# Performance work log

Measured on AMD Instinct MI355X. Metric: run time of the kernel, lower is better.

## Reference

```python
import jax, jax.numpy as jnp
import numpy as np

T, B, C, H, L = 384, 48, 256, 256, 2


def setup_inputs() -> dict:
    key = jax.random.key(0)
    ks = jax.random.split(key, 8)
    s = 1.0 / np.sqrt(H)  # torch GRUCell uniform(-1/sqrt(H), 1/sqrt(H)) init
    xav = np.sqrt(2.0 / (H + 1))  # xavier_normal_ for the [1,H] skip-gate linear
    return {
        "x": jax.random.normal(ks[0], (T, B, C), jnp.float32),
        "hiddens": jax.random.normal(ks[1], (L, 1, H), jnp.float32),
        "w_ih": jax.random.uniform(ks[2], (L, 3 * H, C), jnp.float32, -s, s),
        "w_hh": jax.random.uniform(ks[3], (L, 3 * H, H), jnp.float32, -s, s),
        "b_ih": jax.random.uniform(ks[4], (L, 3 * H), jnp.float32, -s, s),
        "b_hh": jax.random.uniform(ks[5], (L, 3 * H), jnp.float32, -s, s),
        "lw": jax.random.normal(ks[6], (L, 1, H), jnp.float32) * xav,
        "lb": jnp.ones((L, 1), jnp.float32),  # linear.bias.data.fill_(1)
    }


def _ste(v):
    # straight-through round: forward round, backward identity
    return v + jax.lax.stop_gradient(jnp.round(v) - v)


def reference(x, hiddens, w_ih, w_hh, b_ih, b_hh, lw, lb):
    Tn, Bn, _ = x.shape
    Ln, _, Hn = hiddens.shape
    skip = jnp.zeros((Bn,), dtype=bool)          # carried across layers (as in torch loop)
    du = jnp.zeros((Bn, 1), x.dtype)             # delta_u, carried across layers
    inp = x
    hs, bus = [], []
    for i in range(Ln):
        wi, wh, bi, bh = w_ih[i], w_hh[i], b_ih[i], b_hh[i]
        lwi, lbi = lw[i], lb[i]
        h0 = jnp.broadcast_to(hiddens[i], (Bn, Hn))  # h.repeat(1, bs, 1)
        u0 = jnp.ones((Bn, 1), x.dtype)              # u reset per layer

        def step(carry, x_t):
            h, u, skp, d = carry
            bu = _ste(u)                                  # [B,1]
            # GRUCell: gates order (r, z, n)
            gi = x_t @ wi.T + bi                          # [B,3H]
            gh = h @ wh.T + bh                            # [B,3H]
            i_r, i_z, i_n = jnp.split(gi, 3, axis=1)
            h_r, h_z, h_n = jnp.split(gh, 3, axis=1)
            r = jax.nn.sigmoid(i_r + h_r)
            z = jax.nn.sigmoid(i_z + h_z)
            n = jnp.tanh(i_n + r * h_n)
            cand = (1.0 - z) * n + z * h
            # non-skip branch
            h_ns = cand * bu
            d_ns = jax.nn.sigmoid(h_ns @ lwi.T + lbi)     # [B,1]
            s = skp[:, None]
            new_h = jnp.where(s, h * (1.0 - bu), h_ns)
            new_d = jnp.where(s, d, d_ns)
            new_u = jnp.where(s, jnp.clip(u + d, 0.0, 1.0) * (1.0 - bu), d_ns * bu)
            # n_skips_after = ceil(0.5/new_u) - 1 ; skip if > 0 (non-diff path)
            nsa = jnp.ceil(0.5 / jax.lax.stop_gradient(new_u)) - 1.0
            new_skip = nsa[:, 0] > 0
            return (new_h, new_u, new_skip, new_d), (new_h, bu)

        (h_f, _, skip, du), (ys, bu_seq) = jax.lax.scan(step, (h0, u0, skip, du), inp)
        inp = ys                 # [T,B,H] feeds next layer
        hs.append(h_f)           # final hidden [B,H]
        bus.append(bu_seq)       # [T,B,1]
    out = inp
    hs = jnp.stack(hs, axis=0)                                   # [L,B,H]
    total_u = jnp.concatenate([b[:, :, 0].T for b in bus], 1)    # [B, L*T]
    return (out, hs, total_u)
```

## Files before the change

### kernel.cpp

```cpp
#include <hip/hip_runtime.h>
#include <stdint.h>


#define T_STEPS 384
#define BATCH   48
#define HID     256

__device__ __forceinline__ float sigm_(float x) { return 1.f / (1.f + __expf(-x)); }
__device__ __forceinline__ float tanh_(float x) {
    float ax = fabsf(x);
    float e  = __expf(-2.f * ax);
    float r  = (1.f - e) / (1.f + e);
    return copysignf(r, x);
}

__global__ __launch_bounds__(256, 2) void gemm_nt(const float* __restrict__ X,
                                                  const float* __restrict__ W,
                                                  const float* __restrict__ B,
                                                  float* __restrict__ O)
{
    __shared__ float As[32 * 140];
    __shared__ float Bs[32 * 68];

    const int tid = threadIdx.x;
    const int tx  = tid & 15;
    const int ty  = tid >> 4;
    const int n0  = blockIdx.x * 64;
    const int m0  = blockIdx.y * 128;

    float acc[8][4];
#pragma unroll
    for (int i = 0; i < 8; ++i)
#pragma unroll
        for (int j = 0; j < 4; ++j) acc[i][j] = 0.f;

    const float4 bias4 = *reinterpret_cast<const float4*>(B + n0 + tx * 4);

    for (int kc = 0; kc < 8; ++kc) {
        const int k0 = kc * 32;
        float4 a[4], bb[2];
#pragma unroll
        for (int j = 0; j < 4; ++j) {
            int f = tid + 256 * j, r = f >> 3, cq = f & 7;
            a[j] = *reinterpret_cast<const float4*>(X + (size_t)(m0 + r) * 256 + k0 + cq * 4);
        }
#pragma unroll
        for (int j = 0; j < 2; ++j) {
            int f = tid + 256 * j, r = f >> 3, cq = f & 7;
            bb[j] = *reinterpret_cast<const float4*>(W + (size_t)(n0 + r) * 256 + k0 + cq * 4);
        }
        __syncthreads();
#pragma unroll
        for (int j = 0; j < 4; ++j) {
            int f = tid + 256 * j, r = f >> 3, cq = f & 7;
            As[(cq * 4 + 0) * 140 + r] = a[j].x;
            As[(cq * 4 + 1) * 140 + r] = a[j].y;
            As[(cq * 4 + 2) * 140 + r] = a[j].z;
            As[(cq * 4 + 3) * 140 + r] = a[j].w;
        }
#pragma unroll
        for (int j = 0; j < 2; ++j) {
            int f = tid + 256 * j, r = f >> 3, cq = f & 7;
            Bs[(cq * 4 + 0) * 68 + r] = bb[j].x;
            Bs[(cq * 4 + 1) * 68 + r] = bb[j].y;
            Bs[(cq * 4 + 2) * 68 + r] = bb[j].z;
            Bs[(cq * 4 + 3) * 68 + r] = bb[j].w;
        }
        __syncthreads();
#pragma unroll 8
        for (int kk = 0; kk < 32; ++kk) {
            float4 av0 = *reinterpret_cast<const float4*>(As + kk * 140 + ty * 8);
            float4 av1 = *reinterpret_cast<const float4*>(As + kk * 140 + ty * 8 + 4);
            float4 bv  = *reinterpret_cast<const float4*>(Bs + kk * 68 + tx * 4);
            float am[8] = {av0.x, av0.y, av0.z, av0.w, av1.x, av1.y, av1.z, av1.w};
            float bn[4] = {bv.x, bv.y, bv.z, bv.w};
#pragma unroll
            for (int i = 0; i < 8; ++i)
#pragma unroll
                for (int j = 0; j < 4; ++j) acc[i][j] = fmaf(am[i], bn[j], acc[i][j]);
        }
    }
#pragma unroll
    for (int i = 0; i < 8; ++i) {
        int row = m0 + ty * 8 + i;
        float4 o;
        o.x = acc[i][0] + bias4.x;
        o.y = acc[i][1] + bias4.y;
        o.z = acc[i][2] + bias4.z;
        o.w = acc[i][3] + bias4.w;
        *reinterpret_cast<float4*>(O + (size_t)row * 768 + n0 + tx * 4) = o;
    }
}

__global__ __launch_bounds__(512, 2) void rec_layer(
    const float* __restrict__ GI, float* __restrict__ Yout,
    const float* __restrict__ whh, const float* __restrict__ bhh,
    const float* __restrict__ lwl, const float* __restrict__ lbl,
    const float* __restrict__ hid,
    unsigned long long* XH, unsigned long long* PD,
    float* __restrict__ hsout, float* __restrict__ tuout)
{
    __shared__ float hbuf[2112];
    __shared__ float pdw[2][8];

    const int tid  = threadIdx.x;
    const int lane = tid & 63;
    const int w    = tid >> 6;
    const int g    = lane & 15;
    const int s    = lane >> 4;
    const int b    = blockIdx.x % 48;
    const int p    = blockIdx.x / 48;
    const int q    = 1 - p;
    const int cb   = w * 16 + g;
    const int c    = p * 128 + cb;

    float4 WrO[8], WzO[8], WnO[8], WrP[8], WzP[8], WnP[8];
    {
        const size_t rR = (size_t)c * 256;
        const size_t rZ = (size_t)(256 + c) * 256;
        const size_t rN = (size_t)(512 + c) * 256;
        const int ko = p * 128 + s * 32;
        const int kq = q * 128 + s * 32;
        const float4* a  = reinterpret_cast<const float4*>(whh + rR + ko);
        const float4* bv = reinterpret_cast<const float4*>(whh + rZ + ko);
        const float4* cv = reinterpret_cast<const float4*>(whh + rN + ko);
        const float4* d4 = reinterpret_cast<const float4*>(whh + rR + kq);
        const float4* e4 = reinterpret_cast<const float4*>(whh + rZ + kq);
        const float4* f4 = reinterpret_cast<const float4*>(whh + rN + kq);
#pragma unroll
        for (int i = 0; i < 8; ++i) {
            WrO[i] = a[i];  WzO[i] = bv[i]; WnO[i] = cv[i];
            WrP[i] = d4[i]; WzP[i] = e4[i]; WnP[i] = f4[i];
        }
    }

    const float bhr = bhh[c], bhz = bhh[256 + c], bhn = bhh[512 + c];
    const float lwc = lwl[c];
    const float lbv = lbl[0];

    if (tid < 256) {
        float v = hid[tid];
        hbuf[tid] = v; hbuf[264 + tid] = v; hbuf[528 + tid] = v; hbuf[792 + tid] = v;
    }
    __syncthreads();

    float gir, giz, gin;
    {
        const size_t g0 = (size_t)b * 768 + c;
        gir = GI[g0]; giz = GI[g0 + 256]; gin = GI[g0 + 512];
    }
    float sAr, sAz, sAn;
    {
        float ar = 0.f, az = 0.f, an = 0.f;
        const float4* ho = reinterpret_cast<const float4*>(hbuf + s * 264 + p * 128 + s * 32);
        const float4* hq = reinterpret_cast<const float4*>(hbuf + s * 264 + q * 128 + s * 32);
#pragma unroll
        for (int i = 0; i < 8; ++i) {
            float4 hv = ho[i];
            ar = fmaf(WrO[i].x, hv.x, ar); ar = fmaf(WrO[i].y, hv.y, ar);
            ar = fmaf(WrO[i].z, hv.z, ar); ar = fmaf(WrO[i].w, hv.w, ar);
            az = fmaf(WzO[i].x, hv.x, az); az = fmaf(WzO[i].y, hv.y, az);
            az = fmaf(WzO[i].z, hv.z, az); az = fmaf(WzO[i].w, hv.w, az);
            an = fmaf(WnO[i].x, hv.x, an); an = fmaf(WnO[i].y, hv.y, an);
            an = fmaf(WnO[i].z, hv.z, an); an = fmaf(WnO[i].w, hv.w, an);
        }
#pragma unroll
        for (int i = 0; i < 8; ++i) {
            float4 hv = hq[i];
            ar = fmaf(WrP[i].x, hv.x, ar); ar = fmaf(WrP[i].y, hv.y, ar);
            ar = fmaf(WrP[i].z, hv.z, ar); ar = fmaf(WrP[i].w, hv.w, ar);
            az = fmaf(WzP[i].x, hv.x, az); az = fmaf(WzP[i].y, hv.y, az);
            az = fmaf(WzP[i].z, hv.z, az); az = fmaf(WzP[i].w, hv.w, az);
            an = fmaf(WnP[i].x, hv.x, an); an = fmaf(WnP[i].y, hv.y, an);
            an = fmaf(WnP[i].z, hv.z, an); an = fmaf(WnP[i].w, hv.w, an);
        }
        ar += __shfl_xor(ar, 16); ar += __shfl_xor(ar, 32);
        az += __shfl_xor(az, 16); az += __shfl_xor(az, 32);
        an += __shfl_xor(an, 16); an += __shfl_xor(an, 32);
        sAr = ar; sAz = az; sAn = an;
    }

    float u = 1.f, d = 0.f;
    bool  skip = false;
    int   ns = 0;
    int   hp = 0;

    unsigned long long* XHb = XH + b * 512;
    unsigned long long* PDb = PD + b * 4;

    for (int t = 0; t < T_STEPS; ++t) {
        const float bu  = rintf(u);
        const float obu = 1.f - bu;
        const size_t yrow = ((size_t)t * 48 + b) * 256;
        const int tp = (t < T_STEPS - 1) ? t + 1 : t;
        const size_t gpb = ((size_t)tp * 48 + b) * 768 + c;

        if (skip) {
            float* hb = hbuf + hp * 1056;
            float hcv = hb[s * 264 + c];
            float nh  = hcv * obu;
            if (bu != 0.f) hb[s * 264 + c] = nh;
            if (s == 1) {
                Yout[yrow + c] = nh;
                if (t == T_STEPS - 1) hsout[b * 256 + c] = nh;
            }
            if (bu != 0.f) { sAr = 0.f; sAz = 0.f; sAn = 0.f; }
            if (p == 0 && tid == 0) tuout[b * 768 + t] = bu;
            float pr = GI[gpb], pz = GI[gpb + 256], pn = GI[gpb + 512];
            u    = fminf(fmaxf(u + d, 0.f), 1.f) * obu;
            skip = (u < 0.5f);
            __syncthreads();
            gir = pr; giz = pz; gin = pn;
        } else {
            const int sl = ns & 1;
            const unsigned int tag = (unsigned int)ns + 1u;

            float hcv = hbuf[hp * 1056 + s * 264 + c];
            float rr  = sigm_(gir + sAr + bhr);
            float zz  = sigm_(giz + sAz + bhz);
            float tn  = tanh_(gin + rr * (sAn + bhn));
            float nh  = ((1.f - zz) * tn + zz * hcv) * bu;
            float pdv = nh * lwc;

            float* hbn = hbuf + (hp ^ 1) * 1056;
            hbn[s * 264 + c] = nh;
            if (s == 0) {
                unsigned long long pk0p = ((unsigned long long)tag << 32) |
                                          (unsigned long long)__float_as_uint(nh);
                __hip_atomic_store(XHb + sl * 256 + c, pk0p, __ATOMIC_RELAXED, __HIP_MEMORY_SCOPE_AGENT);
            } else if (s == 1) {
                Yout[yrow + c] = nh;
                if (t == T_STEPS - 1) hsout[b * 256 + c] = nh;
            }
            pdv += __shfl_xor(pdv, 1);  pdv += __shfl_xor(pdv, 2);  pdv += __shfl_xor(pdv, 4);
            pdv += __shfl_xor(pdv, 8);  pdv += __shfl_xor(pdv, 16); pdv += __shfl_xor(pdv, 32);
            pdv *= 0.25f;
            if (lane == 0) pdw[sl][w] = pdv;
            if (p == 0 && tid == 0) tuout[b * 768 + t] = bu;
            __syncthreads();

            float ownpd = ((pdw[sl][0] + pdw[sl][1]) + (pdw[sl][2] + pdw[sl][3]))
                        + ((pdw[sl][4] + pdw[sl][5]) + (pdw[sl][6] + pdw[sl][7]));
            if (tid == 0) {
                unsigned long long pkp = ((unsigned long long)tag << 32) |
                                         (unsigned long long)__float_as_uint(ownpd);
                __hip_atomic_store(PDb + sl * 2 + p, pkp, __ATOMIC_RELAXED, __HIP_MEMORY_SCOPE_AGENT);
            }
            unsigned long long pk0 =
                __hip_atomic_load(XHb + sl * 256 + q * 128 + cb, __ATOMIC_RELAXED, __HIP_MEMORY_SCOPE_AGENT);
            float pr = GI[gpb], pz = GI[gpb + 256], pn = GI[gpb + 512];

            float ar = 0.f, az = 0.f, an = 0.f;
            {
                const float4* ho = reinterpret_cast<const float4*>(hbn + s * 264 + p * 128 + s * 32);
#pragma unroll
                for (int i = 0; i < 8; ++i) {
                    float4 hv = ho[i];
                    ar = fmaf(WrO[i].x, hv.x, ar); ar = fmaf(WrO[i].y, hv.y, ar);
                    ar = fmaf(WrO[i].z, hv.z, ar); ar = fmaf(WrO[i].w, hv.w, ar);
                    az = fmaf(WzO[i].x, hv.x, az); az = fmaf(WzO[i].y, hv.y, az);
                    az = fmaf(WzO[i].z, hv.z, az); az = fmaf(WzO[i].w, hv.w, az);
                    an = fmaf(WnO[i].x, hv.x, an); an = fmaf(WnO[i].y, hv.y, an);
                    an = fmaf(WnO[i].z, hv.z, an); an = fmaf(WnO[i].w, hv.w, an);
                }
            }
            {
                const int qc = q * 128 + cb;
                const unsigned long long* slp = XHb + sl * 256 + qc;
                while ((unsigned int)(pk0 >> 32) < tag)
                    pk0 = __hip_atomic_load(slp, __ATOMIC_RELAXED, __HIP_MEMORY_SCOPE_AGENT);
                hbn[s * 264 + qc] = __uint_as_float((unsigned int)pk0);
            }
            __syncthreads();

            unsigned long long pkq = __hip_atomic_load(PDb + sl * 2 + q, __ATOMIC_RELAXED, __HIP_MEMORY_SCOPE_AGENT);

            {
                const float4* hq = reinterpret_cast<const float4*>(hbn + s * 264 + q * 128 + s * 32);
#pragma unroll
                for (int i = 0; i < 8; ++i) {
                    float4 hv = hq[i];
                    ar = fmaf(WrP[i].x, hv.x, ar); ar = fmaf(WrP[i].y, hv.y, ar);
                    ar = fmaf(WrP[i].z, hv.z, ar); ar = fmaf(WrP[i].w, hv.w, ar);
                    az = fmaf(WzP[i].x, hv.x, az); az = fmaf(WzP[i].y, hv.y, az);
                    az = fmaf(WzP[i].z, hv.z, az); az = fmaf(WzP[i].w, hv.w, az);
                    an = fmaf(WnP[i].x, hv.x, an); an = fmaf(WnP[i].y, hv.y, an);
                    an = fmaf(WnP[i].z, hv.z, an); an = fmaf(WnP[i].w, hv.w, an);
                }
            }
            ar += __shfl_xor(ar, 16); ar += __shfl_xor(ar, 32);
            az += __shfl_xor(az, 16); az += __shfl_xor(az, 32);
            an += __shfl_xor(an, 16); an += __shfl_xor(an, 32);
            sAr = ar; sAz = az; sAn = an;

            while ((unsigned int)(pkq >> 32) < tag)
                pkq = __hip_atomic_load(PDb + sl * 2 + q, __ATOMIC_RELAXED, __HIP_MEMORY_SCOPE_AGENT);
            const float pdq = __uint_as_float((unsigned int)pkq);

            float dns = sigm_((ownpd + pdq) + lbv);
            u = dns * bu; d = dns;
            skip = (u < 0.5f);
            ns++; hp ^= 1;
            gir = pr; giz = pz; gin = pn;
        }
    }
}

extern "C" void kernel_launch(void* const* d_in, const int* in_sizes, int n_in,
                              void* d_out, int out_size, void* d_ws, size_t ws_size,
                              hipStream_t stream)
{
    const float* x   = (const float*)d_in[0];
    const float* hid = (const float*)d_in[1];
    const float* wih = (const float*)d_in[2];
    const float* whh = (const float*)d_in[3];
    const float* bih = (const float*)d_in[4];
    const float* bhh = (const float*)d_in[5];
    const float* lw  = (const float*)d_in[6];
    const float* lb  = (const float*)d_in[7];
    float* out = (float*)d_out;

    float* ws = (float*)d_ws;
    float* GI = ws;
    float* Y0 = GI + (size_t)18432 * 768;
    unsigned long long* XH0 = (unsigned long long*)(Y0 + (size_t)18432 * 256);
    unsigned long long* XH1 = XH0 + 48 * 512;
    unsigned long long* PD0 = XH1 + 48 * 512;
    unsigned long long* PD1 = PD0 + 192;

    float* OUTy = out;
    float* HS   = out + (size_t)18432 * 256;
    float* TU   = HS + 2 * 48 * 256;

    hipMemsetAsync(XH0, 0, (size_t)(48 * 512 * 2 + 48 * 4 * 2) * sizeof(unsigned long long), stream);

    dim3 ggrid(12, 144), gblk(256);
    gemm_nt<<<ggrid, gblk, 0, stream>>>(x, wih, bih, GI);
    rec_layer<<<96, 512, 0, stream>>>(GI, Y0, whh, bhh, lw, lb, hid, XH0, PD0, HS, TU);
    gemm_nt<<<ggrid, gblk, 0, stream>>>(Y0, wih + 196608, bih + 768, GI);
    rec_layer<<<96, 512, 0, stream>>>(GI, OUTy, whh + 196608, bhh + 768, lw + 256, lb + 1,
                                      hid + 256, XH1, PD1, HS + 12288, TU + 384);
}
```

Before: 2.064 ms.

## Fuse both GRU layers into one wavefront-pipelined persistent kernel

Replaces the layer-1 recurrence, the layer-2 input GEMM and the layer-2 recurrence with a single persistent launch. Layer-1 blocks stream each hidden state through a 16-slot ring buffer, extra blocks compute the layer-2 input projection per step, and layer-2 blocks consume it, with tag-based atomic flags and progress counters providing flow control. This overlaps the two serial recurrences so their latency chains run concurrently instead of back to back. In exchange it needs all 208 blocks co-resident (risk of deadlock otherwise), adds spin-wait traffic, and computes the layer-2 GEMM per timestep at low efficiency.

```diff
diff --git a/kernel.cpp b/kernel.cpp
--- a/kernel.cpp
+++ b/kernel.cpp
@@ -3,8 +3,7 @@
 
 
 #define T_STEPS 384
-#define BATCH   48
-#define HID     256
+typedef unsigned long long u64t;
 
 __device__ __forceinline__ float sigm_(float x) { return 1.f / (1.f + __expf(-x)); }
 __device__ __forceinline__ float tanh_(float x) {
@@ -92,216 +91,375 @@
     }
 }
 
-__global__ __launch_bounds__(512, 2) void rec_layer(
-    const float* __restrict__ GI, float* __restrict__ Yout,
-    const float* __restrict__ whh, const float* __restrict__ bhh,
-    const float* __restrict__ lwl, const float* __restrict__ lbl,
-    const float* __restrict__ hid,
-    unsigned long long* XH, unsigned long long* PD,
-    float* __restrict__ hsout, float* __restrict__ tuout)
+__global__ __launch_bounds__(512, 2) void fused_pipe(
+    const float* __restrict__ GI1,
+    const float* __restrict__ wih2, const float* __restrict__ bih2,
+    const float* __restrict__ whh1, const float* __restrict__ bhh1,
+    const float* __restrict__ whh2, const float* __restrict__ bhh2,
+    const float* __restrict__ lw1, const float* __restrict__ lb1,
+    const float* __restrict__ lw2, const float* __restrict__ lb2,
+    const float* __restrict__ hid1, const float* __restrict__ hid2,
+    u64t* XH1, u64t* PD1, u64t* XH2, u64t* PD2,
+    u64t* Y1X, u64t* GI2X, unsigned int* BPROG, unsigned int* CPROG,
+    float* __restrict__ OUTy, float* __restrict__ HS, float* __restrict__ TU)
 {
     __shared__ float hbuf[2112];
     __shared__ float pdw[2][8];
+    __shared__ float ybuf[6336];
 
     const int tid  = threadIdx.x;
     const int lane = tid & 63;
     const int w    = tid >> 6;
     const int g    = lane & 15;
     const int s    = lane >> 4;
-    const int b    = blockIdx.x % 48;
-    const int p    = blockIdx.x / 48;
-    const int q    = 1 - p;
-    const int cb   = w * 16 + g;
-    const int c    = p * 128 + cb;
-
-    float4 WrO[8], WzO[8], WnO[8], WrP[8], WzP[8], WnP[8];
-    {
-        const size_t rR = (size_t)c * 256;
-        const size_t rZ = (size_t)(256 + c) * 256;
-        const size_t rN = (size_t)(512 + c) * 256;
-        const int ko = p * 128 + s * 32;
-        const int kq = q * 128 + s * 32;
-        const float4* a  = reinterpret_cast<const float4*>(whh + rR + ko);
-        const float4* bv = reinterpret_cast<const float4*>(whh + rZ + ko);
-        const float4* cv = reinterpret_cast<const float4*>(whh + rN + ko);
-        const float4* d4 = reinterpret_cast<const float4*>(whh + rR + kq);
-        const float4* e4 = reinterpret_cast<const float4*>(whh + rZ + kq);
-        const float4* f4 = reinterpret_cast<const float4*>(whh + rN + kq);
-#pragma unroll
-        for (int i = 0; i < 8; ++i) {
-            WrO[i] = a[i];  WzO[i] = bv[i]; WnO[i] = cv[i];
-            WrP[i] = d4[i]; WzP[i] = e4[i]; WnP[i] = f4[i];
-        }
-    }
-
-    const float bhr = bhh[c], bhz = bhh[256 + c], bhn = bhh[512 + c];
-    const float lwc = lwl[c];
-    const float lbv = lbl[0];
-
-    if (tid < 256) {
-        float v = hid[tid];
-        hbuf[tid] = v; hbuf[264 + tid] = v; hbuf[528 + tid] = v; hbuf[792 + tid] = v;
-    }
-    __syncthreads();
-
-    float gir, giz, gin;
-    {
-        const size_t g0 = (size_t)b * 768 + c;
-        gir = GI[g0]; giz = GI[g0 + 256]; gin = GI[g0 + 512];
-    }
-    float sAr, sAz, sAn;
-    {
-        float ar = 0.f, az = 0.f, an = 0.f;
-        const float4* ho = reinterpret_cast<const float4*>(hbuf + s * 264 + p * 128 + s * 32);
-        const float4* hq = reinterpret_cast<const float4*>(hbuf + s * 264 + q * 128 + s * 32);
-#pragma unroll
-        for (int i = 0; i < 8; ++i) {
-            float4 hv = ho[i];
-            ar = fmaf(WrO[i].x, hv.x, ar); ar = fmaf(WrO[i].y, hv.y, ar);
-            ar = fmaf(WrO[i].z, hv.z, ar); ar = fmaf(WrO[i].w, hv.w, ar);
-            az = fmaf(WzO[i].x, hv.x, az); az = fmaf(WzO[i].y, hv.y, az);
-            az = fmaf(WzO[i].z, hv.z, az); az = fmaf(WzO[i].w, hv.w, az);
-            an = fmaf(WnO[i].x, hv.x, an); an = fmaf(WnO[i].y, hv.y, an);
-            an = fmaf(WnO[i].z, hv.z, an); an = fmaf(WnO[i].w, hv.w, an);
-        }
-#pragma unroll
-        for (int i = 0; i < 8; ++i) {
-            float4 hv = hq[i];
-            ar = fmaf(WrP[i].x, hv.x, ar); ar = fmaf(WrP[i].y, hv.y, ar);
-            ar = fmaf(WrP[i].z, hv.z, ar); ar = fmaf(WrP[i].w, hv.w, ar);
-            az = fmaf(WzP[i].x, hv.x, az); az = fmaf(WzP[i].y, hv.y, az);
-            az = fmaf(WzP[i].z, hv.z, az); az = fmaf(WzP[i].w, hv.w, az);
-            an = fmaf(WnP[i].x, hv.x, an); an = fmaf(WnP[i].y, hv.y, an);
-            an = fmaf(WnP[i].z, hv.z, an); an = fmaf(WnP[i].w, hv.w, an);
-        }
-        ar += __shfl_xor(ar, 16); ar += __shfl_xor(ar, 32);
-        az += __shfl_xor(az, 16); az += __shfl_xor(az, 32);
-        an += __shfl_xor(an, 16); an += __shfl_xor(an, 32);
-        sAr = ar; sAz = az; sAn = an;
-    }
-
-    float u = 1.f, d = 0.f;
-    bool  skip = false;
-    int   ns = 0;
-    int   hp = 0;
-
-    unsigned long long* XHb = XH + b * 512;
-    unsigned long long* PDb = PD + b * 4;
-
-    for (int t = 0; t < T_STEPS; ++t) {
-        const float bu  = rintf(u);
-        const float obu = 1.f - bu;
-        const size_t yrow = ((size_t)t * 48 + b) * 256;
-        const int tp = (t < T_STEPS - 1) ? t + 1 : t;
-        const size_t gpb = ((size_t)tp * 48 + b) * 768 + c;
-
-        if (skip) {
-            float* hb = hbuf + hp * 1056;
-            float hcv = hb[s * 264 + c];
-            float nh  = hcv * obu;
-            if (bu != 0.f) hb[s * 264 + c] = nh;
-            if (s == 1) {
-                Yout[yrow + c] = nh;
-                if (t == T_STEPS - 1) hsout[b * 256 + c] = nh;
-            }
-            if (bu != 0.f) { sAr = 0.f; sAz = 0.f; sAn = 0.f; }
-            if (p == 0 && tid == 0) tuout[b * 768 + t] = bu;
-            float pr = GI[gpb], pz = GI[gpb + 256], pn = GI[gpb + 512];
-            u    = fminf(fmaxf(u + d, 0.f), 1.f) * obu;
-            skip = (u < 0.5f);
-            __syncthreads();
-            gir = pr; giz = pz; gin = pn;
+    const int blk  = blockIdx.x;
+
+    if (blk < 192) {
+        const bool isA = (blk < 96);
+        const int rb   = isA ? blk : (blk - 96);
+        const int b    = rb % 48;
+        const int p    = rb / 48;
+        const int q    = 1 - p;
+        const int cb   = w * 16 + g;
+        const int c    = p * 128 + cb;
+
+        const float* whh = isA ? whh1 : whh2;
+        const float* bhh = isA ? bhh1 : bhh2;
+        const float* lwl = isA ? lw1 : lw2;
+        const float* lbl = isA ? lb1 : lb2;
+        const float* hid = isA ? hid1 : hid2;
+        u64t* XHb = (isA ? XH1 : XH2) + b * 512;
+        u64t* PDb = (isA ? PD1 : PD2) + b * 4;
+
+        float4 WrO[8], WzO[8], WnO[8], WrP[8], WzP[8], WnP[8];
+        {
+            const size_t rR = (size_t)c * 256;
+            const size_t rZ = (size_t)(256 + c) * 256;
+            const size_t rN = (size_t)(512 + c) * 256;
+            const int ko = p * 128 + s * 32;
+            const int kq = q * 128 + s * 32;
+            const float4* a  = reinterpret_cast<const float4*>(whh + rR + ko);
+            const float4* bv = reinterpret_cast<const float4*>(whh + rZ + ko);
+            const float4* cv = reinterpret_cast<const float4*>(whh + rN + ko);
+            const float4* d4 = reinterpret_cast<const float4*>(whh + rR + kq);
+            const float4* e4 = reinterpret_cast<const float4*>(whh + rZ + kq);
+            const float4* f4 = reinterpret_cast<const float4*>(whh + rN + kq);
+#pragma unroll
+            for (int i = 0; i < 8; ++i) {
+                WrO[i] = a[i];  WzO[i] = bv[i]; WnO[i] = cv[i];
+                WrP[i] = d4[i]; WzP[i] = e4[i]; WnP[i] = f4[i];
+            }
+        }
+        const float bhr = bhh[c], bhz = bhh[256 + c], bhn = bhh[512 + c];
+        const float lwc = lwl[c];
+        const float lbv = lbl[0];
+
+        if (tid < 256) {
+            float v = hid[tid];
+            hbuf[tid] = v; hbuf[264 + tid] = v; hbuf[528 + tid] = v; hbuf[792 + tid] = v;
+        }
+        __syncthreads();
+
+        float gir = 0.f, giz = 0.f, gin = 0.f;
+        u64t pkr = 0, pkz = 0, pkn = 0;
+        if (isA) {
+            const size_t g0 = (size_t)b * 768 + c;
+            gir = GI1[g0]; giz = GI1[g0 + 256]; gin = GI1[g0 + 512];
         } else {
-            const int sl = ns & 1;
-            const unsigned int tag = (unsigned int)ns + 1u;
-
-            float hcv = hbuf[hp * 1056 + s * 264 + c];
-            float rr  = sigm_(gir + sAr + bhr);
-            float zz  = sigm_(giz + sAz + bhz);
-            float tn  = tanh_(gin + rr * (sAn + bhn));
-            float nh  = ((1.f - zz) * tn + zz * hcv) * bu;
-            float pdv = nh * lwc;
-
-            float* hbn = hbuf + (hp ^ 1) * 1056;
-            hbn[s * 264 + c] = nh;
-            if (s == 0) {
-                unsigned long long pk0p = ((unsigned long long)tag << 32) |
-                                          (unsigned long long)__float_as_uint(nh);
-                __hip_atomic_store(XHb + sl * 256 + c, pk0p, __ATOMIC_RELAXED, __HIP_MEMORY_SCOPE_AGENT);
-            } else if (s == 1) {
-                Yout[yrow + c] = nh;
-                if (t == T_STEPS - 1) hsout[b * 256 + c] = nh;
-            }
-            pdv += __shfl_xor(pdv, 1);  pdv += __shfl_xor(pdv, 2);  pdv += __shfl_xor(pdv, 4);
-            pdv += __shfl_xor(pdv, 8);  pdv += __shfl_xor(pdv, 16); pdv += __shfl_xor(pdv, 32);
-            pdv *= 0.25f;
-            if (lane == 0) pdw[sl][w] = pdv;
-            if (p == 0 && tid == 0) tuout[b * 768 + t] = bu;
-            __syncthreads();
-
-            float ownpd = ((pdw[sl][0] + pdw[sl][1]) + (pdw[sl][2] + pdw[sl][3]))
-                        + ((pdw[sl][4] + pdw[sl][5]) + (pdw[sl][6] + pdw[sl][7]));
-            if (tid == 0) {
-                unsigned long long pkp = ((unsigned long long)tag << 32) |
-                                         (unsigned long long)__float_as_uint(ownpd);
-                __hip_atomic_store(PDb + sl * 2 + p, pkp, __ATOMIC_RELAXED, __HIP_MEMORY_SCOPE_AGENT);
-            }
-            unsigned long long pk0 =
-                __hip_atomic_load(XHb + sl * 256 + q * 128 + cb, __ATOMIC_RELAXED, __HIP_MEMORY_SCOPE_AGENT);
-            float pr = GI[gpb], pz = GI[gpb + 256], pn = GI[gpb + 512];
-
+            const u64t* g0 = GI2X + ((size_t)b * 16) * 768 + c;
+            pkr = __hip_atomic_load(g0,       __ATOMIC_RELAXED, __HIP_MEMORY_SCOPE_AGENT);
+            pkz = __hip_atomic_load(g0 + 256, __ATOMIC_RELAXED, __HIP_MEMORY_SCOPE_AGENT);
+            pkn = __hip_atomic_load(g0 + 512, __ATOMIC_RELAXED, __HIP_MEMORY_SCOPE_AGENT);
+        }
+
+        float sAr, sAz, sAn;
+        {
             float ar = 0.f, az = 0.f, an = 0.f;
-            {
-                const float4* ho = reinterpret_cast<const float4*>(hbn + s * 264 + p * 128 + s * 32);
-#pragma unroll
-                for (int i = 0; i < 8; ++i) {
-                    float4 hv = ho[i];
-                    ar = fmaf(WrO[i].x, hv.x, ar); ar = fmaf(WrO[i].y, hv.y, ar);
-                    ar = fmaf(WrO[i].z, hv.z, ar); ar = fmaf(WrO[i].w, hv.w, ar);
-                    az = fmaf(WzO[i].x, hv.x, az); az = fmaf(WzO[i].y, hv.y, az);
-                    az = fmaf(WzO[i].z, hv.z, az); az = fmaf(WzO[i].w, hv.w, az);
-                    an = fmaf(WnO[i].x, hv.x, an); an = fmaf(WnO[i].y, hv.y, an);
-                    an = fmaf(WnO[i].z, hv.z, an); an = fmaf(WnO[i].w, hv.w, an);
-                }
-            }
-            {
-                const int qc = q * 128 + cb;
-                const unsigned long long* slp = XHb + sl * 256 + qc;
-                while ((unsigned int)(pk0 >> 32) < tag)
-                    pk0 = __hip_atomic_load(slp, __ATOMIC_RELAXED, __HIP_MEMORY_SCOPE_AGENT);
-                hbn[s * 264 + qc] = __uint_as_float((unsigned int)pk0);
-            }
-            __syncthreads();
-
-            unsigned long long pkq = __hip_atomic_load(PDb + sl * 2 + q, __ATOMIC_RELAXED, __HIP_MEMORY_SCOPE_AGENT);
-
-            {
-                const float4* hq = reinterpret_cast<const float4*>(hbn + s * 264 + q * 128 + s * 32);
-#pragma unroll
-                for (int i = 0; i < 8; ++i) {
-                    float4 hv = hq[i];
-                    ar = fmaf(WrP[i].x, hv.x, ar); ar = fmaf(WrP[i].y, hv.y, ar);
-                    ar = fmaf(WrP[i].z, hv.z, ar); ar = fmaf(WrP[i].w, hv.w, ar);
-                    az = fmaf(WzP[i].x, hv.x, az); az = fmaf(WzP[i].y, hv.y, az);
-                    az = fmaf(WzP[i].z, hv.z, az); az = fmaf(WzP[i].w, hv.w, az);
-                    an = fmaf(WnP[i].x, hv.x, an); an = fmaf(WnP[i].y, hv.y, an);
-                    an = fmaf(WnP[i].z, hv.z, an); an = fmaf(WnP[i].w, hv.w, an);
-                }
+            const float4* ho = reinterpret_cast<const float4*>(hbuf + s * 264 + p * 128 + s * 32);
+            const float4* hq = reinterpret_cast<const float4*>(hbuf + s * 264 + q * 128 + s * 32);
+#pragma unroll
+            for (int i = 0; i < 8; ++i) {
+                float4 hv = ho[i];
+                ar = fmaf(WrO[i].x, hv.x, ar); ar = fmaf(WrO[i].y, hv.y, ar);
+                ar = fmaf(WrO[i].z, hv.z, ar); ar = fmaf(WrO[i].w, hv.w, ar);
+                az = fmaf(WzO[i].x, hv.x, az); az = fmaf(WzO[i].y, hv.y, az);
+                az = fmaf(WzO[i].z, hv.z, az); az = fmaf(WzO[i].w, hv.w, az);
+                an = fmaf(WnO[i].x, hv.x, an); an = fmaf(WnO[i].y, hv.y, an);
+                an = fmaf(WnO[i].z, hv.z, an); an = fmaf(WnO[i].w, hv.w, an);
+            }
+#pragma unroll
+            for (int i = 0; i < 8; ++i) {
+                float4 hv = hq[i];
+                ar = fmaf(WrP[i].x, hv.x, ar); ar = fmaf(WrP[i].y, hv.y, ar);
+                ar = fmaf(WrP[i].z, hv.z, ar); ar = fmaf(WrP[i].w, hv.w, ar);
+                az = fmaf(WzP[i].x, hv.x, az); az = fmaf(WzP[i].y, hv.y, az);
+                az = fmaf(WzP[i].z, hv.z, az); az = fmaf(WzP[i].w, hv.w, az);
+                an = fmaf(WnP[i].x, hv.x, an); an = fmaf(WnP[i].y, hv.y, an);
+                an = fmaf(WnP[i].z, hv.z, an); an = fmaf(WnP[i].w, hv.w, an);
             }
             ar += __shfl_xor(ar, 16); ar += __shfl_xor(ar, 32);
             az += __shfl_xor(az, 16); az += __shfl_xor(az, 32);
             an += __shfl_xor(an, 16); an += __shfl_xor(an, 32);
             sAr = ar; sAz = az; sAn = an;
-
-            while ((unsigned int)(pkq >> 32) < tag)
-                pkq = __hip_atomic_load(PDb + sl * 2 + q, __ATOMIC_RELAXED, __HIP_MEMORY_SCOPE_AGENT);
-            const float pdq = __uint_as_float((unsigned int)pkq);
-
-            float dns = sigm_((ownpd + pdq) + lbv);
-            u = dns * bu; d = dns;
-            skip = (u < 0.5f);
-            ns++; hp ^= 1;
-            gir = pr; giz = pz; gin = pn;
+        }
+
+        float* hsout = isA ? HS : (HS + 12288);
+        float* tubase = TU + (isA ? 0 : 384);
+        u64t*  Y1b = Y1X + (size_t)b * 16 * 256;
+
+        float u = 1.f, d = 0.f;
+        bool  skip = false;
+        int   ns = 0, hp = 0, bcap = 16;
+
+        for (int t = 0; t < T_STEPS; ++t) {
+            const float bu  = rintf(u);
+            const float obu = 1.f - bu;
+            const int tp = (t < T_STEPS - 1) ? t + 1 : t;
+            const size_t gpb = ((size_t)tp * 48 + b) * 768 + c;
+            const u64t* gnext = GI2X + ((size_t)b * 16 + (tp & 15)) * 768 + c;
+            const size_t yrow = ((size_t)t * 48 + b) * 256;
+
+            if (isA && t >= bcap) {
+                unsigned int m;
+                do {
+                    unsigned int p0 = __hip_atomic_load(BPROG + b * 2,     __ATOMIC_RELAXED, __HIP_MEMORY_SCOPE_AGENT);
+                    unsigned int p1 = __hip_atomic_load(BPROG + b * 2 + 1, __ATOMIC_RELAXED, __HIP_MEMORY_SCOPE_AGENT);
+                    m = p0 < p1 ? p0 : p1;
+                } while ((int)m < t - 15);
+                bcap = (int)m + 16;
+            }
+            u64t* yslot = Y1b + (size_t)(t & 15) * 256;
+
+            if (skip) {
+                float* hb = hbuf + hp * 1056;
+                float hcv = hb[s * 264 + c];
+                float nh  = hcv * obu;
+                if (bu != 0.f) hb[s * 264 + c] = nh;
+                if (s == 0) {
+                    if (isA) {
+                        u64t pk = ((u64t)(unsigned)(t + 1) << 32) | (u64t)__float_as_uint(nh);
+                        __hip_atomic_store(yslot + c, pk, __ATOMIC_RELAXED, __HIP_MEMORY_SCOPE_AGENT);
+                    }
+                } else if (s == 1) {
+                    if (!isA) OUTy[yrow + c] = nh;
+                    if (t == T_STEPS - 1) hsout[b * 256 + c] = nh;
+                }
+                if (bu != 0.f) { sAr = 0.f; sAz = 0.f; sAn = 0.f; }
+                if (p == 0 && tid == 0) tubase[b * 768 + t] = bu;
+                if (!isA && tid == 0)
+                    __hip_atomic_store(CPROG + b * 2 + p, (unsigned)(t + 1), __ATOMIC_RELAXED, __HIP_MEMORY_SCOPE_AGENT);
+                float pr = 0.f, pz = 0.f, pn = 0.f;
+                if (isA) { pr = GI1[gpb]; pz = GI1[gpb + 256]; pn = GI1[gpb + 512]; }
+                else {
+                    pkr = __hip_atomic_load(gnext,       __ATOMIC_RELAXED, __HIP_MEMORY_SCOPE_AGENT);
+                    pkz = __hip_atomic_load(gnext + 256, __ATOMIC_RELAXED, __HIP_MEMORY_SCOPE_AGENT);
+                    pkn = __hip_atomic_load(gnext + 512, __ATOMIC_RELAXED, __HIP_MEMORY_SCOPE_AGENT);
+                }
+                u    = fminf(fmaxf(u + d, 0.f), 1.f) * obu;
+                skip = (u < 0.5f);
+                __syncthreads();
+                if (isA) { gir = pr; giz = pz; gin = pn; }
+            } else {
+                const int sl = ns & 1;
+                const unsigned int tag = (unsigned)ns + 1u;
+
+                if (!isA) {
+                    const u64t* gcur = GI2X + ((size_t)b * 16 + (t & 15)) * 768 + c;
+                    const unsigned int wt = (unsigned)(t + 1);
+                    while ((unsigned)(pkr >> 32) < wt)
+                        pkr = __hip_atomic_load(gcur,       __ATOMIC_RELAXED, __HIP_MEMORY_SCOPE_AGENT);
+                    while ((unsigned)(pkz >> 32) < wt)
+                        pkz = __hip_atomic_load(gcur + 256, __ATOMIC_RELAXED, __HIP_MEMORY_SCOPE_AGENT);
+                    while ((unsigned)(pkn >> 32) < wt)
+                        pkn = __hip_atomic_load(gcur + 512, __ATOMIC_RELAXED, __HIP_MEMORY_SCOPE_AGENT);
+                    gir = __uint_as_float((unsigned)pkr);
+                    giz = __uint_as_float((unsigned)pkz);
+                    gin = __uint_as_float((unsigned)pkn);
+                }
+
+                float hcv = hbuf[hp * 1056 + s * 264 + c];
+                float rr  = sigm_(gir + sAr + bhr);
+                float zz  = sigm_(giz + sAz + bhz);
+                float tn  = tanh_(gin + rr * (sAn + bhn));
+                float nh  = ((1.f - zz) * tn + zz * hcv) * bu;
+                float pdv = nh * lwc;
+
+                float* hbn = hbuf + (hp ^ 1) * 1056;
+                hbn[s * 264 + c] = nh;
+                if (s == 0) {
+                    u64t pkx = ((u64t)tag << 32) | (u64t)__float_as_uint(nh);
+                    __hip_atomic_store(XHb + sl * 256 + c, pkx, __ATOMIC_RELAXED, __HIP_MEMORY_SCOPE_AGENT);
+                    if (isA) {
+                        u64t pky = ((u64t)(unsigned)(t + 1) << 32) | (u64t)__float_as_uint(nh);
+                        __hip_atomic_store(yslot + c, pky, __ATOMIC_RELAXED, __HIP_MEMORY_SCOPE_AGENT);
+                    }
+                } else if (s == 1) {
+                    if (!isA) OUTy[yrow + c] = nh;
+                    if (t == T_STEPS - 1) hsout[b * 256 + c] = nh;
+                }
+                pdv += __shfl_xor(pdv, 1);  pdv += __shfl_xor(pdv, 2);  pdv += __shfl_xor(pdv, 4);
+                pdv += __shfl_xor(pdv, 8);  pdv += __shfl_xor(pdv, 16); pdv += __shfl_xor(pdv, 32);
+                pdv *= 0.25f;
+                if (lane == 0) pdw[sl][w] = pdv;
+                if (p == 0 && tid == 0) tubase[b * 768 + t] = bu;
+                if (!isA && tid == 0)
+                    __hip_atomic_store(CPROG + b * 2 + p, (unsigned)(t + 1), __ATOMIC_RELAXED, __HIP_MEMORY_SCOPE_AGENT);
+                __syncthreads();
+
+                float ownpd = ((pdw[sl][0] + pdw[sl][1]) + (pdw[sl][2] + pdw[sl][3]))
+                            + ((pdw[sl][4] + pdw[sl][5]) + (pdw[sl][6] + pdw[sl][7]));
+                if (tid == 0) {
+                    u64t pkp = ((u64t)tag << 32) | (u64t)__float_as_uint(ownpd);
+                    __hip_atomic_store(PDb + sl * 2 + p, pkp, __ATOMIC_RELAXED, __HIP_MEMORY_SCOPE_AGENT);
+                }
+                u64t pk0 = __hip_atomic_load(XHb + sl * 256 + q * 128 + cb, __ATOMIC_RELAXED, __HIP_MEMORY_SCOPE_AGENT);
+                float pr = 0.f, pz = 0.f, pn = 0.f;
+                if (isA) { pr = GI1[gpb]; pz = GI1[gpb + 256]; pn = GI1[gpb + 512]; }
+                else {
+                    pkr = __hip_atomic_load(gnext,       __ATOMIC_RELAXED, __HIP_MEMORY_SCOPE_AGENT);
+                    pkz = __hip_atomic_load(gnext + 256, __ATOMIC_RELAXED, __HIP_MEMORY_SCOPE_AGENT);
+                    pkn = __hip_atomic_load(gnext + 512, __ATOMIC_RELAXED, __HIP_MEMORY_SCOPE_AGENT);
+                }
+
+                float ar = 0.f, az = 0.f, an = 0.f;
+                {
+                    const float4* ho = reinterpret_cast<const float4*>(hbn + s * 264 + p * 128 + s * 32);
+#pragma unroll
+                    for (int i = 0; i < 8; ++i) {
+                        float4 hv = ho[i];
+                        ar = fmaf(WrO[i].x, hv.x, ar); ar = fmaf(WrO[i].y, hv.y, ar);
+                        ar = fmaf(WrO[i].z, hv.z, ar); ar = fmaf(WrO[i].w, hv.w, ar);
+                        az = fmaf(WzO[i].x, hv.x, az); az = fmaf(WzO[i].y, hv.y, az);
+                        az = fmaf(WzO[i].z, hv.z, az); az = fmaf(WzO[i].w, hv.w, az);
+                        an = fmaf(WnO[i].x, hv.x, an); an = fmaf(WnO[i].y, hv.y, an);
+                        an = fmaf(WnO[i].z, hv.z, an); an = fmaf(WnO[i].w, hv.w, an);
+                    }
+                }
+                {
+                    const int qc = q * 128 + cb;
+                    const u64t* slp = XHb + sl * 256 + qc;
+                    while ((unsigned)(pk0 >> 32) < tag)
+                        pk0 = __hip_atomic_load(slp, __ATOMIC_RELAXED, __HIP_MEMORY_SCOPE_AGENT);
+                    hbn[s * 264 + qc] = __uint_as_float((unsigned)pk0);
+                }
+                __syncthreads();
+
+                u64t pkq = __hip_atomic_load(PDb + sl * 2 + q, __ATOMIC_RELAXED, __HIP_MEMORY_SCOPE_AGENT);
+                {
+                    const float4* hq = reinterpret_cast<const float4*>(hbn + s * 264 + q * 128 + s * 32);
+#pragma unroll
+                    for (int i = 0; i < 8; ++i) {
+                        float4 hv = hq[i];
+                        ar = fmaf(WrP[i].x, hv.x, ar); ar = fmaf(WrP[i].y, hv.y, ar);
+                        ar = fmaf(WrP[i].z, hv.z, ar); ar = fmaf(WrP[i].w, hv.w, ar);
+                        az = fmaf(WzP[i].x, hv.x, az); az = fmaf(WzP[i].y, hv.y, az);
+                        az = fmaf(WzP[i].z, hv.z, az); az = fmaf(WzP[i].w, hv.w, az);
+                        an = fmaf(WnP[i].x, hv.x, an); an = fmaf(WnP[i].y, hv.y, an);
+                        an = fmaf(WnP[i].z, hv.z, an); an = fmaf(WnP[i].w, hv.w, an);
+                    }
+                }
+                ar += __shfl_xor(ar, 16); ar += __shfl_xor(ar, 32);
+                az += __shfl_xor(az, 16); az += __shfl_xor(az, 32);
+                an += __shfl_xor(an, 16); an += __shfl_xor(an, 32);
+                sAr = ar; sAz = az; sAn = an;
+
+                while ((unsigned)(pkq >> 32) < tag)
+                    pkq = __hip_atomic_load(PDb + sl * 2 + q, __ATOMIC_RELAXED, __HIP_MEMORY_SCOPE_AGENT);
+                const float pdq = __uint_as_float((unsigned)pkq);
+
+                float dns = sigm_((ownpd + pdq) + lbv);
+                u = dns * bu; d = dns;
+                skip = (u < 0.5f);
+                ns++; hp ^= 1;
+                if (isA) { gir = pr; giz = pz; gin = pn; }
+            }
+        }
+    } else {
+        const int j   = blk - 192;
+        const int hf  = j & 1;
+        const int b0  = (j >> 1) * 6;
+        const int cb2 = w * 16 + g;
+        const int c2  = hf * 128 + cb2;
+
+        float4 Wr[16], Wz[16], Wn[16];
+        {
+            const float4* r4 = reinterpret_cast<const float4*>(wih2 + (size_t)c2 * 256 + s * 64);
+            const float4* z4 = reinterpret_cast<const float4*>(wih2 + (size_t)(256 + c2) * 256 + s * 64);
+            const float4* n4 = reinterpret_cast<const float4*>(wih2 + (size_t)(512 + c2) * 256 + s * 64);
+#pragma unroll
+            for (int i = 0; i < 16; ++i) { Wr[i] = r4[i]; Wz[i] = z4[i]; Wn[i] = n4[i]; }
+        }
+        const float bR = bih2[c2], bZ = bih2[256 + c2], bN = bih2[512 + c2];
+
+        int ccap[6];
+#pragma unroll
+        for (int i = 0; i < 6; ++i) ccap[i] = 16;
+
+        const int i0 = tid, i1 = tid + 512, i2 = tid + 1024;
+        const int bb0 = i0 >> 8, co0 = i0 & 255;
+        const int bb1 = i1 >> 8, co1 = i1 & 255;
+        const int bb2 = i2 >> 8, co2 = i2 & 255;
+
+        for (int t = 0; t < T_STEPS; ++t) {
+            const int slot = t & 15;
+            const unsigned int wt = (unsigned)(t + 1);
+            const u64t* a0 = Y1X + ((size_t)(b0 + bb0) * 16 + slot) * 256 + co0;
+            const u64t* a1 = Y1X + ((size_t)(b0 + bb1) * 16 + slot) * 256 + co1;
+            const u64t* a2 = Y1X + ((size_t)(b0 + bb2) * 16 + slot) * 256 + co2;
+            u64t v0 = __hip_atomic_load(a0, __ATOMIC_RELAXED, __HIP_MEMORY_SCOPE_AGENT);
+            u64t v1 = __hip_atomic_load(a1, __ATOMIC_RELAXED, __HIP_MEMORY_SCOPE_AGENT);
+            u64t v2 = __hip_atomic_load(a2, __ATOMIC_RELAXED, __HIP_MEMORY_SCOPE_AGENT);
+            while ((unsigned)(v0 >> 32) < wt) v0 = __hip_atomic_load(a0, __ATOMIC_RELAXED, __HIP_MEMORY_SCOPE_AGENT);
+            while ((unsigned)(v1 >> 32) < wt) v1 = __hip_atomic_load(a1, __ATOMIC_RELAXED, __HIP_MEMORY_SCOPE_AGENT);
+            while ((unsigned)(v2 >> 32) < wt) v2 = __hip_atomic_load(a2, __ATOMIC_RELAXED, __HIP_MEMORY_SCOPE_AGENT);
+            {
+                float v = __uint_as_float((unsigned)v0); float* yb = ybuf + bb0 * 1056;
+                yb[co0] = v; yb[264 + co0] = v; yb[528 + co0] = v; yb[792 + co0] = v;
+            }
+            {
+                float v = __uint_as_float((unsigned)v1); float* yb = ybuf + bb1 * 1056;
+                yb[co1] = v; yb[264 + co1] = v; yb[528 + co1] = v; yb[792 + co1] = v;
+            }
+            {
+                float v = __uint_as_float((unsigned)v2); float* yb = ybuf + bb2 * 1056;
+                yb[co2] = v; yb[264 + co2] = v; yb[528 + co2] = v; yb[792 + co2] = v;
+            }
+            __syncthreads();
+            if (tid < 6)
+                __hip_atomic_store(BPROG + (b0 + tid) * 2 + hf, wt, __ATOMIC_RELAXED, __HIP_MEMORY_SCOPE_AGENT);
+#pragma unroll
+            for (int bb = 0; bb < 6; ++bb) {
+                if (t >= ccap[bb]) {
+                    unsigned int m;
+                    do {
+                        m = __hip_atomic_load(CPROG + (b0 + bb) * 2 + hf, __ATOMIC_RELAXED, __HIP_MEMORY_SCOPE_AGENT);
+                    } while ((int)m < t - 15);
+                    ccap[bb] = (int)m + 16;
+                }
+                float ar = 0.f, az = 0.f, an = 0.f;
+                const float4* yv = reinterpret_cast<const float4*>(ybuf + bb * 1056 + s * 328);
+#pragma unroll
+                for (int i = 0; i < 16; ++i) {
+                    float4 hv = yv[i];
+                    ar = fmaf(Wr[i].x, hv.x, ar); ar = fmaf(Wr[i].y, hv.y, ar);
+                    ar = fmaf(Wr[i].z, hv.z, ar); ar = fmaf(Wr[i].w, hv.w, ar);
+                    az = fmaf(Wz[i].x, hv.x, az); az = fmaf(Wz[i].y, hv.y, az);
+                    az = fmaf(Wz[i].z, hv.z, az); az = fmaf(Wz[i].w, hv.w, az);
+                    an = fmaf(Wn[i].x, hv.x, an); an = fmaf(Wn[i].y, hv.y, an);
+                    an = fmaf(Wn[i].z, hv.z, an); an = fmaf(Wn[i].w, hv.w, an);
+                }
+                ar += __shfl_xor(ar, 16); ar += __shfl_xor(ar, 32);
+                az += __shfl_xor(az, 16); az += __shfl_xor(az, 32);
+                an += __shfl_xor(an, 16); an += __shfl_xor(an, 32);
+                ar += bR; az += bZ; an += bN;
+                if (s < 3) {
+                    float v = (s == 0) ? ar : ((s == 1) ? az : an);
+                    u64t pk = ((u64t)wt << 32) | (u64t)__float_as_uint(v);
+                    __hip_atomic_store(GI2X + ((size_t)(b0 + bb) * 16 + slot) * 768 + s * 256 + c2,
+                                       pk, __ATOMIC_RELAXED, __HIP_MEMORY_SCOPE_AGENT);
+                }
+            }
+            __syncthreads();
         }
     }
 }
@@ -322,22 +480,28 @@
 
     float* ws = (float*)d_ws;
     float* GI = ws;
-    float* Y0 = GI + (size_t)18432 * 768;
-    unsigned long long* XH0 = (unsigned long long*)(Y0 + (size_t)18432 * 256);
-    unsigned long long* XH1 = XH0 + 48 * 512;
-    unsigned long long* PD0 = XH1 + 48 * 512;
-    unsigned long long* PD1 = PD0 + 192;
+    u64t* XH1 = (u64t*)(GI + (size_t)18432 * 768);
+    u64t* XH2 = XH1 + 24576;
+    u64t* PD1 = XH2 + 24576;
+    u64t* PD2 = PD1 + 192;
+    u64t* Y1X = PD2 + 192;
+    u64t* GI2X = Y1X + 196608;
+    unsigned int* BPROG = (unsigned int*)(GI2X + 589824);
+    unsigned int* CPROG = BPROG + 96;
 
     float* OUTy = out;
     float* HS   = out + (size_t)18432 * 256;
     float* TU   = HS + 2 * 48 * 256;
 
-    hipMemsetAsync(XH0, 0, (size_t)(48 * 512 * 2 + 48 * 4 * 2) * sizeof(unsigned long long), stream);
+    hipMemsetAsync(XH1, 0, (size_t)835968 * sizeof(u64t) + 768, stream);
 
     dim3 ggrid(12, 144), gblk(256);
     gemm_nt<<<ggrid, gblk, 0, stream>>>(x, wih, bih, GI);
-    rec_layer<<<96, 512, 0, stream>>>(GI, Y0, whh, bhh, lw, lb, hid, XH0, PD0, HS, TU);
-    gemm_nt<<<ggrid, gblk, 0, stream>>>(Y0, wih + 196608, bih + 768, GI);
-    rec_layer<<<96, 512, 0, stream>>>(GI, OUTy, whh + 196608, bhh + 768, lw + 256, lb + 1,
-                                      hid + 256, XH1, PD1, HS + 12288, TU + 384);
+    fused_pipe<<<208, 512, 0, stream>>>(GI,
+        wih + 196608, bih + 768,
+        whh, bhh, whh + 196608, bhh + 768,
+        lw, lb, lw + 256, lb + 1,
+        hid, hid + 256,
+        XH1, PD1, XH2, PD2, Y1X, GI2X, BPROG, CPROG,
+        OUTy, HS, TU);
 }
```

Result: faster. 1.986 ms (-3.8%).
